# Kernel optimization log

Hardware: AMD Instinct MI355X
Metric: run time of the kernel (lower is better)

The kernel has to match this reference:

```python
import jax, jax.numpy as jnp
import numpy as np

T, B = 1024, 16384
GAMMA = 0.99
LAMBDA = 0.97


def setup_inputs() -> dict:
    key = jax.random.key(0)
    k1, k2 = jax.random.split(key)
    value = jax.random.normal(k1, (T + 1, B), dtype=jnp.float32)
    reward = jax.random.normal(k2, (T, B), dtype=jnp.float32)
    return {"value": value, "reward": reward}


def reference(value, reward):
    # delta[t] = r[t] + gamma * V[t+1] - V[t]          shape (T, B)
    delta = reward + GAMMA * value[1:] - value[:-1]
    coef = jnp.float32(GAMMA * LAMBDA)

    def step(carry, d):
        adv_t = d + coef * carry
        return adv_t, adv_t

    init = jnp.zeros(delta.shape[1:], dtype=delta.dtype)
    # reverse-in-time scan: adv[t] = delta[t] + gamma*lambda * adv[t+1]
    _, adv = jax.lax.scan(step, init, delta, reverse=True)
    return adv
```

## Files before the change

kernel.cpp:

```cpp
#include <hip/hip_runtime.h>


constexpr int T_ = 1024;
constexpr int B_ = 16384;
constexpr float GAMMA = 0.99f;
constexpr float COEF  = (float)(0.99 * 0.97);

__host__ __device__ constexpr float pow_coef(int n) {
    float p = 1.0f;
    for (int i = 0; i < n; ++i) p *= COEF;
    return p;
}

typedef float f32x4 __attribute__((ext_vector_type(4)));

static __device__ __forceinline__ void store_nt(float* p, float4 v) {
    f32x4 nv = {v.x, v.y, v.z, v.w};
    __builtin_nontemporal_store(nv, (f32x4*)p);
}

template<int L>
__global__ __launch_bounds__(256) void gae_sum(
    const float* __restrict__ value,
    const float* __restrict__ reward,
    float* __restrict__ S)
{
    const int c4    = blockIdx.x * 256 + threadIdx.x;
    const int chunk = blockIdx.y;
    const size_t b  = (size_t)c4 * 4;
    const int t0    = chunk * L;

    float4 v[L + 1];
    float4 r[L];
    #pragma unroll
    for (int i = 0; i <= L; ++i)
        v[i] = *(const float4*)(value + (size_t)(t0 + i) * B_ + b);
    #pragma unroll
    for (int i = 0; i < L; ++i)
        r[i] = *(const float4*)(reward + (size_t)(t0 + i) * B_ + b);

    float4 s = make_float4(0.f, 0.f, 0.f, 0.f);
    #pragma unroll
    for (int i = L - 1; i >= 0; --i) {
        s.x = (r[i].x + GAMMA * v[i + 1].x - v[i].x) + COEF * s.x;
        s.y = (r[i].y + GAMMA * v[i + 1].y - v[i].y) + COEF * s.y;
        s.z = (r[i].z + GAMMA * v[i + 1].z - v[i].z) + COEF * s.z;
        s.w = (r[i].w + GAMMA * v[i + 1].w - v[i].w) + COEF * s.w;
    }
    *(float4*)(S + (size_t)chunk * B_ + b) = s;
}

template<int L>
__global__ __launch_bounds__(256) void gae_out(
    const float* __restrict__ value,
    const float* __restrict__ reward,
    const float* __restrict__ S,
    float* __restrict__ out)
{
    constexpr int C = T_ / L;
    constexpr float CL = pow_coef(L);

    const int c4    = blockIdx.x * 256 + threadIdx.x;
    const int chunk = blockIdx.y;
    const size_t b  = (size_t)c4 * 4;
    const int t0    = chunk * L;

    float4 v[L + 1];
    float4 r[L];
    #pragma unroll
    for (int i = 0; i <= L; ++i)
        v[i] = *(const float4*)(value + (size_t)(t0 + i) * B_ + b);
    #pragma unroll
    for (int i = 0; i < L; ++i)
        r[i] = *(const float4*)(reward + (size_t)(t0 + i) * B_ + b);

    float4 a = make_float4(0.f, 0.f, 0.f, 0.f);
    for (int j = C - 1; j > chunk; --j) {
        float4 s = *(const float4*)(S + (size_t)j * B_ + b);
        a.x = s.x + CL * a.x;
        a.y = s.y + CL * a.y;
        a.z = s.z + CL * a.z;
        a.w = s.w + CL * a.w;
    }

    #pragma unroll
    for (int i = L - 1; i >= 0; --i) {
        a.x = (r[i].x + GAMMA * v[i + 1].x - v[i].x) + COEF * a.x;
        a.y = (r[i].y + GAMMA * v[i + 1].y - v[i].y) + COEF * a.y;
        a.z = (r[i].z + GAMMA * v[i + 1].z - v[i].z) + COEF * a.z;
        a.w = (r[i].w + GAMMA * v[i + 1].w - v[i].w) + COEF * a.w;
        store_nt(out + (size_t)(t0 + i) * B_ + b, a);
    }
}

extern "C" void kernel_launch(void* const* d_in, const int* in_sizes, int n_in,
                              void* d_out, int out_size, void* d_ws, size_t ws_size,
                              hipStream_t stream) {
    const float* value  = (const float*)d_in[0];
    const float* reward = (const float*)d_in[1];
    float* out = (float*)d_out;
    float* S   = (float*)d_ws;

    dim3 block(256);

    if (ws_size >= (size_t)(T_ / 8) * B_ * sizeof(float)) {
        dim3 grid(B_ / 4 / 256, T_ / 8);
        gae_sum<8><<<grid, block, 0, stream>>>(value, reward, S);
        gae_out<8><<<grid, block, 0, stream>>>(value, reward, S, out);
    } else {
        dim3 grid(B_ / 4 / 256, T_ / 16);
        gae_sum<16><<<grid, block, 0, stream>>>(value, reward, S);
        gae_out<16><<<grid, block, 0, stream>>>(value, reward, S, out);
    }
}
```

Measured before the change: 198.8 us.

## Add carry-propagation kernel to replace per-chunk quadratic reduction of chunk sums

Adds a middle kernel that runs the exclusive reverse scan over the per-chunk partial sums once per column and writes each chunk's incoming carry back into the workspace. The output kernel then loads a single carry value instead of looping over all later chunk sums, which was quadratic work and repeated reads of S. It also adds empty inline-asm register pins so all loads are issued before the compute, aiming to raise memory-level parallelism. The cost is an extra kernel launch and a serial 128-element loop per column in the carry kernel.

```diff
diff --git a/kernel.cpp b/kernel.cpp
--- a/kernel.cpp
+++ b/kernel.cpp
@@ -19,6 +19,10 @@
     __builtin_nontemporal_store(nv, (f32x4*)p);
 }
 
+static __device__ __forceinline__ void pin(const float4& f) {
+    asm volatile("" :: "v"(f.x), "v"(f.y), "v"(f.z), "v"(f.w));
+}
+
 template<int L>
 __global__ __launch_bounds__(256) void gae_sum(
     const float* __restrict__ value,
@@ -38,6 +42,10 @@
     #pragma unroll
     for (int i = 0; i < L; ++i)
         r[i] = *(const float4*)(reward + (size_t)(t0 + i) * B_ + b);
+    #pragma unroll
+    for (int i = 0; i <= L; ++i) pin(v[i]);
+    #pragma unroll
+    for (int i = 0; i < L; ++i) pin(r[i]);
 
     float4 s = make_float4(0.f, 0.f, 0.f, 0.f);
     #pragma unroll
@@ -50,6 +58,28 @@
     *(float4*)(S + (size_t)chunk * B_ + b) = s;
 }
 
+template<int C>
+__global__ __launch_bounds__(256) void gae_carry(float* __restrict__ S)
+{
+    constexpr float CL = pow_coef(T_ / C);
+    const int col = blockIdx.x * 256 + threadIdx.x;
+
+    float s[C];
+    #pragma unroll
+    for (int j = 0; j < C; ++j)
+        s[j] = S[(size_t)j * B_ + col];
+    #pragma unroll
+    for (int j = 0; j < C; ++j)
+        asm volatile("" :: "v"(s[j]));
+
+    float run = 0.f;
+    #pragma unroll
+    for (int j = C - 1; j >= 0; --j) {
+        S[(size_t)j * B_ + col] = run;
+        run = s[j] + CL * run;
+    }
+}
+
 template<int L>
 __global__ __launch_bounds__(256) void gae_out(
     const float* __restrict__ value,
@@ -57,14 +87,12 @@
     const float* __restrict__ S,
     float* __restrict__ out)
 {
-    constexpr int C = T_ / L;
-    constexpr float CL = pow_coef(L);
-
     const int c4    = blockIdx.x * 256 + threadIdx.x;
     const int chunk = blockIdx.y;
     const size_t b  = (size_t)c4 * 4;
     const int t0    = chunk * L;
 
+    float4 carry = *(const float4*)(S + (size_t)chunk * B_ + b);
     float4 v[L + 1];
     float4 r[L];
     #pragma unroll
@@ -73,16 +101,13 @@
     #pragma unroll
     for (int i = 0; i < L; ++i)
         r[i] = *(const float4*)(reward + (size_t)(t0 + i) * B_ + b);
+    pin(carry);
+    #pragma unroll
+    for (int i = 0; i <= L; ++i) pin(v[i]);
+    #pragma unroll
+    for (int i = 0; i < L; ++i) pin(r[i]);
 
-    float4 a = make_float4(0.f, 0.f, 0.f, 0.f);
-    for (int j = C - 1; j > chunk; --j) {
-        float4 s = *(const float4*)(S + (size_t)j * B_ + b);
-        a.x = s.x + CL * a.x;
-        a.y = s.y + CL * a.y;
-        a.z = s.z + CL * a.z;
-        a.w = s.w + CL * a.w;
-    }
-
+    float4 a = carry;
     #pragma unroll
     for (int i = L - 1; i >= 0; --i) {
         a.x = (r[i].x + GAMMA * v[i + 1].x - v[i].x) + COEF * a.x;
@@ -102,14 +127,17 @@
     float* S   = (float*)d_ws;
 
     dim3 block(256);
+    dim3 gridC(B_ / 256);
 
     if (ws_size >= (size_t)(T_ / 8) * B_ * sizeof(float)) {
         dim3 grid(B_ / 4 / 256, T_ / 8);
-        gae_sum<8><<<grid, block, 0, stream>>>(value, reward, S);
-        gae_out<8><<<grid, block, 0, stream>>>(value, reward, S, out);
+        gae_sum<8>  <<<grid,  block, 0, stream>>>(value, reward, S);
+        gae_carry<T_/8><<<gridC, block, 0, stream>>>(S);
+        gae_out<8>  <<<grid,  block, 0, stream>>>(value, reward, S, out);
     } else {
         dim3 grid(B_ / 4 / 256, T_ / 16);
-        gae_sum<16><<<grid, block, 0, stream>>>(value, reward, S);
-        gae_out<16><<<grid, block, 0, stream>>>(value, reward, S, out);
+        gae_sum<16> <<<grid,  block, 0, stream>>>(value, reward, S);
+        gae_carry<T_/16><<<gridC, block, 0, stream>>>(S);
+        gae_out<16> <<<grid,  block, 0, stream>>>(value, reward, S, out);
     }
 }
```

Result: faster. 189.7 us (-4.6%).
